# Performance work log

Measured on AMD Instinct MI355X. Metric: run time of the kernel, lower is better.

The kernel has to match this reference:

```python
import jax, jax.numpy as jnp
import numpy as np
from jax import lax

THR = 0.0
NMS_SIZE = 5
PAD = NMS_SIZE // 2
B, C, H, W = 8, 1, 2048, 2048
# Upper bound on number of surviving peaks: ~1/(2*25) of pixels pass in
# expectation for iid noise; B*H*W//8 is a very safe static cap.
MAX_PEAKS = (B * H * W) // 8


def max_filter(x):
    # torch MaxPool2d(kernel=5, stride=1, padding=2) == max reduce_window
    # with -inf padding, same spatial output shape.
    return lax.reduce_window(
        x, -jnp.inf, lax.max,
        window_dimensions=(1, 1, NMS_SIZE, NMS_SIZE),
        window_strides=(1, 1, 1, 1),
        padding=[(0, 0), (0, 0), (PAD, PAD), (PAD, PAD)],
    )


def setup_inputs() -> dict:
    key = jax.random.key(0)
    scores = jax.random.normal(key, (B, C, H, W), dtype=jnp.float32)
    return {"scores": scores}


def reference(scores):
    # maxima = (scores == maxpool(scores)) & (scores > thr)
    maxima = (scores == max_filter(scores)) & (scores > THR)
    # torch: maxima.nonzero().t()[2:4] -> [2, K] rows = (h, w) coords.
    # jit-safe: fixed-size nonzero, padded with -1 for absent entries.
    idx = jnp.nonzero(maxima, size=MAX_PEAKS, fill_value=-1)
    return jnp.stack([idx[2], idx[3]])  # [2, MAX_PEAKS]
```

## Files before the change

kernel.cpp:

```cpp
#include <hip/hip_runtime.h>
#include <math.h>

#define IMG_W 2048
#define IMG_H 2048
#define BATCH 8
#define MAX_PEAKS ((BATCH * IMG_H * IMG_W) / 8)
#define NWORDS (BATCH * IMG_H * IMG_W / 32)
#define ROWSW 32
#define NFILL 2048

__global__ __launch_bounds__(256) void nms_mask(const float* __restrict__ scores,
                                                unsigned* __restrict__ words,
                                                unsigned* __restrict__ bsum) {
    const int t = threadIdx.x;
    const int lane = t & 63;
    const int wv = t >> 6;
    const int b = blockIdx.x;
    const int img = b >> 7;
    const int rem = b & 127;
    const int strip = rem >> 4;
    const int chunk = rem & 15;
    const int r0 = chunk * 128 + wv * ROWSW;
    const int c0 = strip * 256;
    const int cl = c0 + lane * 4;
    const long imgBase = (long)img * (IMG_H * IMG_W);

    const float* colp = scores + imgBase + cl;
    const bool isL = (lane == 0), isR = (lane == 63);
    const int ecol = isL ? (c0 - 4) : (c0 + 256);
    const bool evalid = (isL || isR) && ((unsigned)ecol < IMG_W);
    const float* ecolp = scores + imgBase + ecol;

    const float NEG = -INFINITY;
    float4 ring[8];
    float2 ringE[8];

#pragma unroll
    for (int m = 0; m < 4; ++m) {
        int gr = r0 - 2 + m;
        float4 nv = make_float4(NEG, NEG, NEG, NEG);
        float2 ne = make_float2(NEG, NEG);
        if ((unsigned)gr < IMG_H) {
            nv = *(const float4*)(colp + (long)gr * IMG_W);
            if (evalid) {
                float4 ev = *(const float4*)(ecolp + (long)gr * IMG_W);
                ne = isL ? make_float2(ev.z, ev.w) : make_float2(ev.x, ev.y);
            }
        }
        ring[m] = nv;
        ringE[m] = ne;
    }

    unsigned cnt = 0;
    const int shamt = (lane & 7) * 4;
    long wIdx = (long)(img * IMG_H + r0) * (IMG_W / 32) + strip * 8 + (lane >> 3);
    const int cb0 = (img * IMG_H + r0) >> 4;

#pragma unroll 1
    for (int i8 = 0; i8 < ROWSW / 8; ++i8) {
#pragma unroll
        for (int u = 0; u < 8; ++u) {
            const int gr = r0 + i8 * 8 + u + 2;
            float4 nv = make_float4(NEG, NEG, NEG, NEG);
            float2 ne = make_float2(NEG, NEG);
            if ((unsigned)gr < IMG_H) {
                nv = *(const float4*)(colp + (long)gr * IMG_W);
                if (evalid) {
                    float4 ev = *(const float4*)(ecolp + (long)gr * IMG_W);
                    ne = isL ? make_float2(ev.z, ev.w) : make_float2(ev.x, ev.y);
                }
            }
            ring[(u + 4) & 7] = nv;
            ringE[(u + 4) & 7] = ne;

            const float4 w0 = ring[u & 7];
            const float4 w1 = ring[(u + 1) & 7];
            const float4 mid = ring[(u + 2) & 7];
            const float4 w3 = ring[(u + 3) & 7];
            const float4 w4 = ring[(u + 4) & 7];
            float vmx = fmaxf(fmaxf(fmaxf(w0.x, w1.x), fmaxf(mid.x, w3.x)), w4.x);
            float vmy = fmaxf(fmaxf(fmaxf(w0.y, w1.y), fmaxf(mid.y, w3.y)), w4.y);
            float vmz = fmaxf(fmaxf(fmaxf(w0.z, w1.z), fmaxf(mid.z, w3.z)), w4.z);
            float vmw = fmaxf(fmaxf(fmaxf(w0.w, w1.w), fmaxf(mid.w, w3.w)), w4.w);
            const float2 e0 = ringE[u & 7];
            const float2 e1 = ringE[(u + 1) & 7];
            const float2 e2 = ringE[(u + 2) & 7];
            const float2 e3 = ringE[(u + 3) & 7];
            const float2 e4 = ringE[(u + 4) & 7];
            float vex = fmaxf(fmaxf(fmaxf(e0.x, e1.x), fmaxf(e2.x, e3.x)), e4.x);
            float vey = fmaxf(fmaxf(fmaxf(e0.y, e1.y), fmaxf(e2.y, e3.y)), e4.y);

            float A = __shfl_up(vmz, 1);
            float B = __shfl_up(vmw, 1);
            float C = __shfl_down(vmx, 1);
            float D = __shfl_down(vmy, 1);
            if (isL) { A = vex; B = vey; }
            if (isR) { C = vex; D = vey; }

            float t12 = fmaxf(vmy, vmz);
            float m02 = fmaxf(vmx, t12);
            float m03 = fmaxf(m02, vmw);
            float m13 = fmaxf(t12, vmw);
            float h0 = fmaxf(fmaxf(A, B), m02);
            float h1 = fmaxf(B, m03);
            float h2 = fmaxf(m03, C);
            float h3 = fmaxf(m13, fmaxf(C, D));

            unsigned nib = 0;
            nib |= (mid.x > 0.0f && mid.x >= h0) ? 1u : 0u;
            nib |= (mid.y > 0.0f && mid.y >= h1) ? 2u : 0u;
            nib |= (mid.z > 0.0f && mid.z >= h2) ? 4u : 0u;
            nib |= (mid.w > 0.0f && mid.w >= h3) ? 8u : 0u;

            unsigned wd = nib << shamt;
            wd |= __shfl_xor(wd, 1);
            wd |= __shfl_xor(wd, 2);
            wd |= __shfl_xor(wd, 4);
            if ((lane & 7) == 0) {
                words[wIdx] = wd;
                cnt += __popc(wd);
            }
            wIdx += IMG_W / 32;
        }
        if (i8 & 1) {
            unsigned s = cnt;
            s += __shfl_xor(s, 1);
            s += __shfl_xor(s, 2);
            s += __shfl_xor(s, 4);
            s += __shfl_xor(s, 8);
            s += __shfl_xor(s, 16);
            s += __shfl_xor(s, 32);
            if (lane == 0) atomicAdd(&bsum[cb0 + (i8 >> 1)], s);
            cnt = 0;
        }
    }
}

__global__ __launch_bounds__(256) void nms_scan(const unsigned* __restrict__ bsum,
                                                unsigned* __restrict__ base) {
    __shared__ unsigned wtot[4];
    const int t = threadIdx.x;
    const int lane = t & 63, wid = t >> 6;
    uint4 v = ((const uint4*)bsum)[t];
    unsigned s0 = v.x, s1 = v.x + v.y, s2 = s1 + v.z, ts = s2 + v.w;
    unsigned sc = ts;
#pragma unroll
    for (int d = 1; d < 64; d <<= 1) {
        unsigned o = __shfl_up(sc, d);
        if (lane >= d) sc += o;
    }
    if (lane == 63) wtot[wid] = sc;
    __syncthreads();
    unsigned wpre = 0;
#pragma unroll
    for (int k = 0; k < 4; ++k) wpre += (k < wid) ? wtot[k] : 0u;
    unsigned excl = wpre + sc - ts;
    ((uint4*)base)[t] = make_uint4(excl, excl + s0, excl + s1, excl + s2);
    if (t == 255) base[1024] = wpre + sc;
}

__global__ __launch_bounds__(256) void nms_compact(const unsigned* __restrict__ words,
                                                   const unsigned* __restrict__ base,
                                                   int* __restrict__ out) {
    const int t = threadIdx.x;
    const int b = blockIdx.x;
    if (b < 1024) {
        __shared__ unsigned wq[4];
        const int lane = t & 63, wid = t >> 6;
        uint4 q = ((const uint4*)(words + b * 1024))[t];
        unsigned wv[4] = {q.x, q.y, q.z, q.w};
        unsigned tsum = __popc(wv[0]) + __popc(wv[1]) + __popc(wv[2]) + __popc(wv[3]);
        unsigned sc = tsum;
#pragma unroll
        for (int d = 1; d < 64; d <<= 1) {
            unsigned o = __shfl_up(sc, d);
            if (lane >= d) sc += o;
        }
        if (lane == 63) wq[wid] = sc;
        __syncthreads();
        unsigned wpre = 0;
#pragma unroll
        for (int k = 0; k < 4; ++k) wpre += (k < wid) ? wq[k] : 0u;
        unsigned off = base[b] + wpre + sc - tsum;

        const unsigned gword0 = (unsigned)b * 1024u + (unsigned)t * 4u;
#pragma unroll
        for (int wi = 0; wi < 4; ++wi) {
            unsigned m = wv[wi];
            unsigned pbase = (gword0 + wi) << 5;
            while (m) {
                int bit = __builtin_ctz(m);
                m &= m - 1;
                unsigned ppix = pbase + (unsigned)bit;
                int hh = (int)((ppix >> 11) & 2047u);
                int ww = (int)(ppix & 2047u);
                if (off < (unsigned)MAX_PEAKS) {
                    out[off] = hh;
                    out[MAX_PEAKS + off] = ww;
                }
                ++off;
            }
        }
    } else {
        unsigned total = base[1024];
        if (total > (unsigned)MAX_PEAKS) total = MAX_PEAKS;
        unsigned tail = (unsigned)MAX_PEAKS - total;
        unsigned fb = (unsigned)(b - 1024);
        unsigned per = (tail + NFILL - 1) / NFILL;
        unsigned s = total + fb * per;
        unsigned e = s + per;
        if (e > (unsigned)MAX_PEAKS) e = MAX_PEAKS;
        for (unsigned k = s + t; k < e; k += 256) {
            out[k] = -1;
            out[MAX_PEAKS + k] = -1;
        }
    }
}

extern "C" void kernel_launch(void* const* d_in, const int* in_sizes, int n_in,
                              void* d_out, int out_size, void* d_ws, size_t ws_size,
                              hipStream_t stream) {
    const float* scores = (const float*)d_in[0];
    int* out = (int*)d_out;
    unsigned* words = (unsigned*)d_ws;
    unsigned* bsum = words + NWORDS;
    unsigned* base = bsum + 1024;

    hipMemsetAsync(bsum, 0, 1024 * sizeof(unsigned), stream);
    nms_mask<<<1024, 256, 0, stream>>>(scores, words, bsum);
    nms_scan<<<1, 256, 0, stream>>>(bsum, base);
    nms_compact<<<1024 + NFILL, 256, 0, stream>>>(words, base, out);
}
```

Baseline: 216.7 us.

## Replace atomic chunk counts with per-strip slots, drop memset, branchless edge loads

Each wave now writes its chunk popcount to a dedicated slot indexed by chunk and strip instead of using atomicAdd into a shared counter. That removes the hipMemsetAsync launch and the atomic contention, and the scan kernel sums the 8 strip slots per chunk itself. Row loads become branchless: row indices are clamped, all lanes load a halo column, and invalid values are masked with selects. This trades extra redundant halo loads for less divergence. Launch bounds also gain an occupancy hint of 4 blocks per SM.

```diff
diff --git a/kernel.cpp b/kernel.cpp
--- a/kernel.cpp
+++ b/kernel.cpp
@@ -9,9 +9,30 @@
 #define ROWSW 32
 #define NFILL 2048
 
-__global__ __launch_bounds__(256) void nms_mask(const float* __restrict__ scores,
-                                                unsigned* __restrict__ words,
-                                                unsigned* __restrict__ bsum) {
+__device__ __forceinline__ void load_row(const float* __restrict__ colp,
+                                         const float* __restrict__ ecolp,
+                                         int gr, bool leftHalf, bool evalid,
+                                         float4& nv, float2& ne) {
+    const float NEG = -INFINITY;
+    int rc = gr < 0 ? 0 : (gr > IMG_H - 1 ? IMG_H - 1 : gr);
+    size_t off = (size_t)rc * IMG_W;
+    float4 v = *(const float4*)(colp + off);
+    float4 ev = *(const float4*)(ecolp + off);
+    bool rv = ((unsigned)gr < IMG_H);
+    bool ok = rv && evalid;
+    float ex = leftHalf ? ev.z : ev.x;
+    float ey = leftHalf ? ev.w : ev.y;
+    nv.x = rv ? v.x : NEG;
+    nv.y = rv ? v.y : NEG;
+    nv.z = rv ? v.z : NEG;
+    nv.w = rv ? v.w : NEG;
+    ne.x = ok ? ex : NEG;
+    ne.y = ok ? ey : NEG;
+}
+
+__global__ __launch_bounds__(256, 4) void nms_mask(const float* __restrict__ scores,
+                                                   unsigned* __restrict__ words,
+                                                   unsigned* __restrict__ bsum2) {
     const int t = threadIdx.x;
     const int lane = t & 63;
     const int wv = t >> 6;
@@ -23,37 +44,26 @@
     const int r0 = chunk * 128 + wv * ROWSW;
     const int c0 = strip * 256;
     const int cl = c0 + lane * 4;
-    const long imgBase = (long)img * (IMG_H * IMG_W);
+    const size_t imgBase = (size_t)img * (IMG_H * IMG_W);
 
     const float* colp = scores + imgBase + cl;
+    const bool leftHalf = (lane < 32);
     const bool isL = (lane == 0), isR = (lane == 63);
-    const int ecol = isL ? (c0 - 4) : (c0 + 256);
-    const bool evalid = (isL || isR) && ((unsigned)ecol < IMG_W);
-    const float* ecolp = scores + imgBase + ecol;
-
-    const float NEG = -INFINITY;
+    int ecol = leftHalf ? (c0 - 4) : (c0 + 256);
+    const bool evalid = ((unsigned)ecol < IMG_W);
+    int ecolC = evalid ? ecol : c0;
+    const float* ecolp = scores + imgBase + ecolC;
+
     float4 ring[8];
     float2 ringE[8];
 
 #pragma unroll
-    for (int m = 0; m < 4; ++m) {
-        int gr = r0 - 2 + m;
-        float4 nv = make_float4(NEG, NEG, NEG, NEG);
-        float2 ne = make_float2(NEG, NEG);
-        if ((unsigned)gr < IMG_H) {
-            nv = *(const float4*)(colp + (long)gr * IMG_W);
-            if (evalid) {
-                float4 ev = *(const float4*)(ecolp + (long)gr * IMG_W);
-                ne = isL ? make_float2(ev.z, ev.w) : make_float2(ev.x, ev.y);
-            }
-        }
-        ring[m] = nv;
-        ringE[m] = ne;
-    }
+    for (int m = 0; m < 4; ++m)
+        load_row(colp, ecolp, r0 - 2 + m, leftHalf, evalid, ring[m], ringE[m]);
 
     unsigned cnt = 0;
     const int shamt = (lane & 7) * 4;
-    long wIdx = (long)(img * IMG_H + r0) * (IMG_W / 32) + strip * 8 + (lane >> 3);
+    size_t wIdx = (size_t)(img * IMG_H + r0) * (IMG_W / 32) + strip * 8 + (lane >> 3);
     const int cb0 = (img * IMG_H + r0) >> 4;
 
 #pragma unroll 1
@@ -61,17 +71,8 @@
 #pragma unroll
         for (int u = 0; u < 8; ++u) {
             const int gr = r0 + i8 * 8 + u + 2;
-            float4 nv = make_float4(NEG, NEG, NEG, NEG);
-            float2 ne = make_float2(NEG, NEG);
-            if ((unsigned)gr < IMG_H) {
-                nv = *(const float4*)(colp + (long)gr * IMG_W);
-                if (evalid) {
-                    float4 ev = *(const float4*)(ecolp + (long)gr * IMG_W);
-                    ne = isL ? make_float2(ev.z, ev.w) : make_float2(ev.x, ev.y);
-                }
-            }
-            ring[(u + 4) & 7] = nv;
-            ringE[(u + 4) & 7] = ne;
+            load_row(colp, ecolp, gr, leftHalf, evalid,
+                     ring[(u + 4) & 7], ringE[(u + 4) & 7]);
 
             const float4 w0 = ring[u & 7];
             const float4 w1 = ring[(u + 1) & 7];
@@ -130,19 +131,25 @@
             s += __shfl_xor(s, 8);
             s += __shfl_xor(s, 16);
             s += __shfl_xor(s, 32);
-            if (lane == 0) atomicAdd(&bsum[cb0 + (i8 >> 1)], s);
+            if (lane == 0) bsum2[(cb0 + (i8 >> 1)) * 8 + strip] = s;
             cnt = 0;
         }
     }
 }
 
-__global__ __launch_bounds__(256) void nms_scan(const unsigned* __restrict__ bsum,
+__global__ __launch_bounds__(256) void nms_scan(const unsigned* __restrict__ bsum2,
                                                 unsigned* __restrict__ base) {
     __shared__ unsigned wtot[4];
     const int t = threadIdx.x;
     const int lane = t & 63, wid = t >> 6;
-    uint4 v = ((const uint4*)bsum)[t];
-    unsigned s0 = v.x, s1 = v.x + v.y, s2 = s1 + v.z, ts = s2 + v.w;
+    const uint4* p = (const uint4*)(bsum2 + t * 32);
+    unsigned c[4];
+#pragma unroll
+    for (int i = 0; i < 4; ++i) {
+        uint4 a = p[2 * i], bq = p[2 * i + 1];
+        c[i] = a.x + a.y + a.z + a.w + bq.x + bq.y + bq.z + bq.w;
+    }
+    unsigned s0 = c[0], s1 = s0 + c[1], s2 = s1 + c[2], ts = s2 + c[3];
     unsigned sc = ts;
 #pragma unroll
     for (int d = 1; d < 64; d <<= 1) {
@@ -223,11 +230,10 @@
     const float* scores = (const float*)d_in[0];
     int* out = (int*)d_out;
     unsigned* words = (unsigned*)d_ws;
-    unsigned* bsum = words + NWORDS;
-    unsigned* base = bsum + 1024;
-
-    hipMemsetAsync(bsum, 0, 1024 * sizeof(unsigned), stream);
-    nms_mask<<<1024, 256, 0, stream>>>(scores, words, bsum);
-    nms_scan<<<1, 256, 0, stream>>>(bsum, base);
+    unsigned* bsum2 = words + NWORDS;
+    unsigned* base = bsum2 + 8192;
+
+    nms_mask<<<1024, 256, 0, stream>>>(scores, words, bsum2);
+    nms_scan<<<1, 256, 0, stream>>>(bsum2, base);
     nms_compact<<<1024 + NFILL, 256, 0, stream>>>(words, base, out);
 }
```

Result: no change. 213.7 us (-1.4%).
